# Performance work log

Hardware: AMD Instinct MI355X
Metric: run time of the kernel (lower is better)

## Reference

```python
import jax, jax.numpy as jnp
import numpy as np

ACT_BITS = 8
W_BITS = 8
BN_EPS = 1e-5


def _round_ste(x):
    # straight-through round (HAWQ-style ste_round)
    return x + jax.lax.stop_gradient(jnp.round(x) - x)


def _quant_sym(x, bits):
    # symmetric per-tensor fake quantization; scale treated as constant (EMA min/max in original)
    n = float(2 ** (bits - 1) - 1)
    s = jax.lax.stop_gradient(jnp.maximum(jnp.max(jnp.abs(x)) / n, 1e-8))
    xq = jnp.clip(_round_ste(x / s), -n - 1.0, n) * s
    return xq, s


def _conv(x, w, stride, pad):
    return jax.lax.conv_general_dilated(
        x, w, (stride, stride), [(pad, pad), (pad, pad)],
        dimension_numbers=("NCHW", "OIHW", "NCHW"))


def _quant_bn(x, gamma, beta, mean, var):
    # fold BN into a per-channel scale+bias; quantize the folded scale like a weight
    ws = gamma * jax.lax.rsqrt(var + BN_EPS)          # [C]
    wq, ws_scale = _quant_sym(ws, W_BITS)
    b = beta - mean * wq                               # [C]
    return x * wq[None, :, None, None] + b[None, :, None, None], ws_scale


def setup_inputs() -> dict:
    key = jax.random.key(0)
    ks = jax.random.split(key, 16)
    d = {}
    d["x"] = jax.random.normal(ks[0], (32, 128, 56, 56), jnp.float32)
    d["w1"] = jax.random.normal(ks[1], (256, 128, 3, 3), jnp.float32) * 0.05
    d["w2"] = jax.random.normal(ks[2], (256, 256, 3, 3), jnp.float32) * 0.05
    d["w_id"] = jax.random.normal(ks[3], (256, 128, 1, 1), jnp.float32) * 0.05
    for i, pfx in enumerate(["bn1", "bn2", "id"]):
        k4 = jax.random.split(ks[4 + i], 4)
        d[pfx + "_gamma"] = jax.random.uniform(k4[0], (256,), jnp.float32) + 0.5
        d[pfx + "_beta"] = jax.random.normal(k4[1], (256,), jnp.float32) * 0.1
        d[pfx + "_mean"] = jax.random.normal(k4[2], (256,), jnp.float32) * 0.1
        d[pfx + "_var"] = jax.random.uniform(k4[3], (256,), jnp.float32) + 0.5
    return d


def reference(x, w1, w2, w_id,
              bn1_gamma, bn1_beta, bn1_mean, bn1_var,
              bn2_gamma, bn2_beta, bn2_mean, bn2_var,
              id_gamma, id_beta, id_mean, id_var):
    # quant_act on block input
    xq, act_s = _quant_sym(x, ACT_BITS)

    # identity branch: 1x1 stride-2 quantized conv -> quant_act -> folded quant bn
    w_id_q, _ = _quant_sym(w_id, W_BITS)
    identity = _conv(xq, w_id_q, 2, 0)
    identity, _ = _quant_sym(identity, ACT_BITS)
    identity, _ = _quant_bn(identity, id_gamma, id_beta, id_mean, id_var)

    # main branch conv1 (3x3 stride 2) -> act quant -> bn -> relu -> act quant
    w1_q, _ = _quant_sym(w1, W_BITS)
    h = _conv(xq, w1_q, 2, 1)
    h, _ = _quant_sym(h, ACT_BITS)
    h, _ = _quant_bn(h, bn1_gamma, bn1_beta, bn1_mean, bn1_var)
    h = jax.nn.relu(h)
    h, _ = _quant_sym(h, ACT_BITS)

    # conv2 (3x3 stride 1) -> act quant -> bn
    w2_q, _ = _quant_sym(w2, W_BITS)
    h = _conv(h, w2_q, 1, 1)
    h, _ = _quant_sym(h, ACT_BITS)
    h, _ = _quant_bn(h, bn2_gamma, bn2_beta, bn2_mean, bn2_var)

    # residual add -> int32 requant -> relu
    h = h + identity
    h, out_s = _quant_sym(h, ACT_BITS)
    h = jax.nn.relu(h)
    return h, out_s
```

## Files before the change

kernel.cpp:

```cpp
#include <hip/hip_runtime.h>
#include <limits.h>

#define THREADS 256
#define GRID_BLOCKS 896

typedef int vi4 __attribute__((ext_vector_type(4)));

__device__ __forceinline__ float clamp8f(float q) { return fminf(fmaxf(q, -128.0f), 127.0f); }
__device__ __forceinline__ float sc_from_bits(unsigned b) {
  return fmaxf(__uint_as_float(b) / 127.0f, 1e-8f);
}
__device__ __forceinline__ signed char q8(float v, float s) {
  return (signed char)(int)clamp8f(rintf(v / s));
}


__device__ __forceinline__ void gbar(int* IS, int base, int bx, int subTgt) {
  asm volatile("s_waitcnt vmcnt(0)" ::: "memory");
  int old = __hip_atomic_fetch_add(IS + base + (bx & 7) * 16, 1, __ATOMIC_RELAXED,
                                   __HIP_MEMORY_SCOPE_AGENT);
  if (old == subTgt - 1) {
    int r = __hip_atomic_fetch_add(IS + base + 128, 1, __ATOMIC_RELAXED, __HIP_MEMORY_SCOPE_AGENT);
    if (r == 7)
      __hip_atomic_fetch_add(IS + base + 144, 1, __ATOMIC_RELAXED, __HIP_MEMORY_SCOPE_AGENT);
  }
  while (__hip_atomic_load(IS + base + 144, __ATOMIC_RELAXED, __HIP_MEMORY_SCOPE_SYSTEM) == 0)
    __builtin_amdgcn_s_sleep(2);
}

__device__ __forceinline__ void amax_body(const float4* __restrict__ p, int n4, int bid,
                                          int nblocks, int* __restrict__ slot) {
  const int tid = threadIdx.x;
  const int stride = nblocks * THREADS;
  float m = 0.0f;
  int i = bid * THREADS + tid;
  for (; i + 3 * stride < n4; i += 4 * stride) {
    float4 v0 = p[i];
    float4 v1 = p[i + stride];
    float4 v2 = p[i + 2 * stride];
    float4 v3 = p[i + 3 * stride];
    float m0 = fmaxf(fmaxf(fabsf(v0.x), fabsf(v0.y)), fmaxf(fabsf(v0.z), fabsf(v0.w)));
    float m1 = fmaxf(fmaxf(fabsf(v1.x), fabsf(v1.y)), fmaxf(fabsf(v1.z), fabsf(v1.w)));
    float m2 = fmaxf(fmaxf(fabsf(v2.x), fabsf(v2.y)), fmaxf(fabsf(v2.z), fabsf(v2.w)));
    float m3 = fmaxf(fmaxf(fabsf(v3.x), fabsf(v3.y)), fmaxf(fabsf(v3.z), fabsf(v3.w)));
    m = fmaxf(m, fmaxf(fmaxf(m0, m1), fmaxf(m2, m3)));
  }
  for (; i < n4; i += stride) {
    float4 v = p[i];
    m = fmaxf(m, fmaxf(fmaxf(fabsf(v.x), fabsf(v.y)), fmaxf(fabsf(v.z), fabsf(v.w))));
  }
#pragma unroll
  for (int k = 32; k >= 1; k >>= 1) m = fmaxf(m, __shfl_xor(m, k));
  __shared__ float wred[4];
  if ((tid & 63) == 0) wred[tid >> 6] = m;
  __syncthreads();
  if (tid == 0) {
    m = fmaxf(fmaxf(wred[0], wred[1]), fmaxf(wred[2], wred[3]));
    atomicMax(slot, __float_as_int(m));
  }
}

__device__ __forceinline__ float sc_slot(const int* IS, int slot) {
  unsigned u = (unsigned)__hip_atomic_load((int*)(IS + slot), __ATOMIC_RELAXED,
                                           __HIP_MEMORY_SCOPE_AGENT);
  return fmaxf(__uint_as_float(u) / 127.0f, 1e-8f);
}

__global__ __launch_bounds__(THREADS, 8) void k_pq(
    int* IS, const float* g1, const float* be1, const float* m1, const float* v1, float* wq1,
    float* b1, const float* g2, const float* be2, const float* m2, const float* v2, float* wq2,
    float* b2, const float* gi, const float* bei, const float* mi, const float* vvi, float* wqi,
    float* bi, const float* x, int* X8, const float* w1f, vi4* W1m, const float* w2f, vi4* W2m,
    const float* widf, vi4* Widm) {
  __shared__ signed char tile[56 * 132];
  __shared__ float red[THREADS];
  const int bx = blockIdx.x;
  const int t = threadIdx.x;

  {
    int b = bx;
    if (b < 3) {
      const float *gamma, *beta, *mean, *var;
      float *wq, *bb;
      if (b == 0) { gamma = g1; beta = be1; mean = m1; var = v1; wq = wq1; bb = b1; }
      else if (b == 1) { gamma = g2; beta = be2; mean = m2; var = v2; wq = wq2; bb = b2; }
      else { gamma = gi; beta = bei; mean = mi; var = vvi; wq = wqi; bb = bi; }
      int c = t;
      float ws = gamma[c] * (1.0f / sqrtf(var[c] + 1e-5f));
      red[c] = fabsf(ws);
      __syncthreads();
      for (int s = THREADS / 2; s > 0; s >>= 1) {
        if (c < s) red[c] = fmaxf(red[c], red[c + s]);
        __syncthreads();
      }
      float sws = fmaxf(red[0] / 127.0f, 1e-8f);
      float q = clamp8f(rintf(ws / sws)) * sws;
      wq[c] = q;
      bb[c] = beta[c] - mean[c] * q;
    } else {
      b -= 3;
      if (b < 64) {
        amax_body((const float4*)w1f, 73728, b, 64, IS + 1);
      } else {
        b -= 64;
        if (b < 128) {
          amax_body((const float4*)w2f, 147456, b, 128, IS + 2);
        } else {
          b -= 128;
          if (b < 16) amax_body((const float4*)widf, 8192, b, 16, IS + 3);
          else amax_body((const float4*)x, 3211264, b - 16, 1805, IS + 0);
        }
      }
    }
  }
  __syncthreads();
  if (t == 0) gbar(IS, 128, bx, 252);
  __syncthreads();

  int b = bx;
  if (b < 1792) {
    float s = sc_slot(IS, 0);
    int h = b % 56, n = b / 56;
    const float* xp = x + ((n * 128) * 56 + h) * 56;
#pragma unroll
    for (int k = 0; k < 28; ++k) {
      int i = t + k * 256;
      int w = i % 56, c = i / 56;
      tile[w * 132 + c] = q8(xp[c * 3136 + w], s);
    }
    __syncthreads();
    int* op = X8 + (n * 56 + h) * 56 * 32;
#pragma unroll
    for (int k = 0; k < 7; ++k) {
      int i = t + k * 256;
      int w = i >> 5, c4 = (i & 31) * 4;
      const signed char* tp = tile + w * 132 + c4;
      op[i] = (int)(unsigned char)tp[0] | ((int)(unsigned char)tp[1] << 8) |
              ((int)(unsigned char)tp[2] << 16) | ((int)(unsigned char)tp[3] << 24);
    }
    return;
  }
  if (b < 1864) {
    int tt = (b - 1792) * THREADS + t;
    float s = sc_slot(IS, 1);
    int lane = tt & 63;
    int cotile = (tt >> 6) & 15;
    int ks = tt >> 10;
    int tap = ks >> 1, kc = ks & 1;
    int kh = tap / 3, kw = tap % 3;
    int co = cotile * 16 + (lane & 15);
    int ci0 = kc * 64 + (lane >> 4) * 16;
    const float* src = w1f + (co * 128 + ci0) * 9 + kh * 3 + kw;
    int r[4];
#pragma unroll
    for (int q = 0; q < 4; ++q) {
      unsigned b0 = (unsigned char)q8(src[(q * 4 + 0) * 9], s);
      unsigned b1v = (unsigned char)q8(src[(q * 4 + 1) * 9], s);
      unsigned b2v = (unsigned char)q8(src[(q * 4 + 2) * 9], s);
      unsigned b3 = (unsigned char)q8(src[(q * 4 + 3) * 9], s);
      r[q] = (int)(b0 | (b1v << 8) | (b2v << 16) | (b3 << 24));
    }
    vi4 v = {r[0], r[1], r[2], r[3]};
    W1m[tt] = v;
    return;
  }
  if (b < 2008) {
    int tt = (b - 1864) * THREADS + t;
    float s = sc_slot(IS, 2);
    int lane = tt & 63;
    int cotile = (tt >> 6) & 15;
    int ks = tt >> 10;
    int tap = ks >> 2, kc = ks & 3;
    int kh = tap / 3, kw = tap % 3;
    int co = cotile * 16 + (lane & 15);
    int ci0 = kc * 64 + (lane >> 4) * 16;
    const float* src = w2f + (co * 256 + ci0) * 9 + kh * 3 + kw;
    int r[4];
#pragma unroll
    for (int q = 0; q < 4; ++q) {
      unsigned b0 = (unsigned char)q8(src[(q * 4 + 0) * 9], s);
      unsigned b1v = (unsigned char)q8(src[(q * 4 + 1) * 9], s);
      unsigned b2v = (unsigned char)q8(src[(q * 4 + 2) * 9], s);
      unsigned b3 = (unsigned char)q8(src[(q * 4 + 3) * 9], s);
      r[q] = (int)(b0 | (b1v << 8) | (b2v << 16) | (b3 << 24));
    }
    vi4 v = {r[0], r[1], r[2], r[3]};
    W2m[tt] = v;
    return;
  }
  {
    int tt = (b - 2008) * THREADS + t;
    float s = sc_slot(IS, 3);
    int lane = tt & 63;
    int cotile = (tt >> 6) & 15;
    int ks = tt >> 10;
    int co = cotile * 16 + (lane & 15);
    int ci0 = ks * 64 + (lane >> 4) * 16;
    const float* src = widf + co * 128 + ci0;
    int r[4];
#pragma unroll
    for (int q = 0; q < 4; ++q) {
      unsigned b0 = (unsigned char)q8(src[q * 4 + 0], s);
      unsigned b1v = (unsigned char)q8(src[q * 4 + 1], s);
      unsigned b2v = (unsigned char)q8(src[q * 4 + 2], s);
      unsigned b3 = (unsigned char)q8(src[q * 4 + 3], s);
      r[q] = (int)(b0 | (b1v << 8) | (b2v << 16) | (b3 << 24));
    }
    vi4 v = {r[0], r[1], r[2], r[3]};
    Widm[tt] = v;
  }
}

#define MFMA_I8(a, b, c) __builtin_amdgcn_mfma_i32_16x16x64_i8(a, b, c, 0, 0, 0)

__device__ __forceinline__ signed char qact(int v, float sxw, float s_h1, float s_y2, float wq,
                                            float bb) {
  float hf = (float)v * sxw;
  float q = clamp8f(rintf(hf / s_h1));
  float hv = q * s_h1;
  float y = fmaxf(hv * wq + bb, 0.0f);
  float a = fminf(fmaxf(rintf(y / s_y2), -128.0f), 127.0f);
  return (signed char)(int)a;
}

__global__ __launch_bounds__(THREADS, 4) void k_cv1(const int* X8, const vi4* __restrict__ W1m,
                                                    const vi4* __restrict__ Widm,
                                                    int* __restrict__ IDI, int* A2i, int* IS,
                                                    const float* __restrict__ wq1,
                                                    const float* __restrict__ b1, float* SC) {
  __shared__ __align__(16) int lds[9280];
  __shared__ int redA[4], redB[4];
  __shared__ float redF[4];
  __shared__ float sSxw, sSh1, sSy2;
  const int tid = threadIdx.x;
  const int bx = blockIdx.x;
  const int n = bx / 28, rr = bx % 28;
  const int hp = rr >> 1, nh = rr & 1;
  const int ho0 = hp * 2;
  vi4 zero = {0, 0, 0, 0};

  for (int r = 0; r < 5; ++r) {
    int h = 2 * ho0 - 1 + r;
    int* dst = lds + r * 58 * 32;
    if (h >= 0 && h < 56) {
      const vi4* src = (const vi4*)(X8 + (n * 56 + h) * 56 * 32);
      for (int i4 = tid; i4 < 448; i4 += THREADS) {
        int col = i4 >> 3, e0 = (i4 & 7) * 4;
        int cell = r * 58 + col + 1;
        *(vi4*)(lds + cell * 32 + (e0 ^ ((cell & 7) << 2))) = src[i4];
      }
      if (tid < 32) dst[tid] = 0;
      else if (tid >= 128 && tid < 160) dst[57 * 32 + (tid - 128)] = 0;
    } else {
      for (int i4 = tid; i4 < 464; i4 += THREADS) ((vi4*)dst)[i4] = zero;
    }
  }
  __syncthreads();

  const int lane = tid & 63, wv = tid >> 6;
  const int mw = wv & 1, nw = wv >> 1;
  const int lm = lane & 15, quad = lane >> 4;
  const int woc0 = lm, woc1 = (16 + lm) > 27 ? 27 : (16 + lm);
  const int choff = quad * 4;
  const int ho = ho0 + mw;
  const int obase = ((n * 28 + ho) * 28) * 256;
  const int ctbase = nh * 8 + nw * 4;

#define LDA(row, colp, sub)                                                              \
  (*(const vi4*)(lds + ((row) * 58 + (colp)) * 32 +                                      \
                 ((sub) ^ ((((row) * 58 + (colp)) & 7) << 2))))

  vi4 acc[2][4];
  vi4 bA[4], bB[4];
  vi4 a0A, a1A, a0B, a1B;

#pragma unroll
  for (int mt = 0; mt < 2; ++mt)
#pragma unroll
    for (int ct = 0; ct < 4; ++ct) acc[mt][ct] = zero;
  const vi4* wibase = Widm + ctbase * 64 + lane;
  {
    const int row = 2 * mw + 1;
#pragma unroll
    for (int kc = 0; kc < 2; ++kc) {
      vi4 a0 = LDA(row, 2 * woc0 + 1, kc * 16 + choff);
      vi4 a1 = LDA(row, 2 * woc1 + 1, kc * 16 + choff);
#pragma unroll
      for (int ct = 0; ct < 4; ++ct) {
        vi4 b = wibase[kc * 1024 + ct * 64];
        acc[0][ct] = MFMA_I8(a0, b, acc[0][ct]);
        acc[1][ct] = MFMA_I8(a1, b, acc[1][ct]);
      }
    }
  }
  int am = 0;
#pragma unroll
  for (int ct = 0; ct < 4; ++ct) {
    const int co = (ctbase + ct) * 16 + lm;
#pragma unroll
    for (int mt = 0; mt < 2; ++mt)
#pragma unroll
      for (int r = 0; r < 4; ++r) {
        int wo = mt * 16 + quad * 4 + r;
        if (wo < 28) {
          int v = acc[mt][ct][r];
          IDI[obase + wo * 256 + co] = v;
          am = max(am, v < 0 ? -v : v);
        }
      }
  }
#pragma unroll
  for (int k = 32; k >= 1; k >>= 1) am = max(am, __shfl_xor(am, k));
  if (lane == 0) redA[wv] = am;

#pragma unroll
  for (int mt = 0; mt < 2; ++mt)
#pragma unroll
    for (int ct = 0; ct < 4; ++ct) acc[mt][ct] = zero;
  const vi4* wbase = W1m + ctbase * 64 + lane;
#pragma unroll
  for (int ct = 0; ct < 4; ++ct) bA[ct] = wbase[ct * 64];
  {
    a0A = LDA(2 * mw, 2 * woc0, choff);
    a1A = LDA(2 * mw, 2 * woc1, choff);
  }
#pragma unroll 1
  for (int ks = 0; ks < 18; ks += 2) {
    {
      const int ksn = ks + 1;
      const int khn = (ksn >= 6) + (ksn >= 12);
      const int t2 = ksn - khn * 6;
      const int kwn = t2 >> 1, kcn = t2 & 1;
#pragma unroll
      for (int ct = 0; ct < 4; ++ct) bB[ct] = wbase[ksn * 1024 + ct * 64];
      const int row = 2 * mw + khn;
      a0B = LDA(row, 2 * woc0 + kwn, kcn * 16 + choff);
      a1B = LDA(row, 2 * woc1 + kwn, kcn * 16 + choff);
    }
#pragma unroll
    for (int ct = 0; ct < 4; ++ct) {
      acc[0][ct] = MFMA_I8(a0A, bA[ct], acc[0][ct]);
      acc[1][ct] = MFMA_I8(a1A, bA[ct], acc[1][ct]);
    }
    if (ks + 2 < 18) {
      const int ksn = ks + 2;
      const int khn = (ksn >= 6) + (ksn >= 12);
      const int t2 = ksn - khn * 6;
      const int kwn = t2 >> 1, kcn = t2 & 1;
#pragma unroll
      for (int ct = 0; ct < 4; ++ct) bA[ct] = wbase[ksn * 1024 + ct * 64];
      const int row = 2 * mw + khn;
      a0A = LDA(row, 2 * woc0 + kwn, kcn * 16 + choff);
      a1A = LDA(row, 2 * woc1 + kwn, kcn * 16 + choff);
    }
#pragma unroll
    for (int ct = 0; ct < 4; ++ct) {
      acc[0][ct] = MFMA_I8(a0B, bB[ct], acc[0][ct]);
      acc[1][ct] = MFMA_I8(a1B, bB[ct], acc[1][ct]);
    }
  }

  int vmx[4], vmn[4];
  int am1 = 0;
#pragma unroll
  for (int ct = 0; ct < 4; ++ct) {
    int vmax = INT_MIN, vmin = INT_MAX;
#pragma unroll
    for (int mt = 0; mt < 2; ++mt)
#pragma unroll
      for (int r = 0; r < 4; ++r) {
        int wo = mt * 16 + quad * 4 + r;
        if (wo < 28) {
          int v = acc[mt][ct][r];
          vmax = max(vmax, v);
          vmin = min(vmin, v);
        }
      }
    vmax = max(vmax, __shfl_xor(vmax, 16));
    vmax = max(vmax, __shfl_xor(vmax, 32));
    vmin = min(vmin, __shfl_xor(vmin, 16));
    vmin = min(vmin, __shfl_xor(vmin, 32));
    vmx[ct] = vmax;
    vmn[ct] = vmin;
    am1 = max(am1, max(vmax < 0 ? -vmax : vmax, vmin < 0 ? -vmin : vmin));
  }
#pragma unroll
  for (int k = 8; k >= 1; k >>= 1) am1 = max(am1, __shfl_xor(am1, k));
  if (lane == 0) redB[wv] = am1;

  __syncthreads();
#pragma unroll
  for (int ct = 0; ct < 4; ++ct) {
    const int cl = (nw * 4 + ct) * 16 + lm;
#pragma unroll
    for (int mt = 0; mt < 2; ++mt)
#pragma unroll
      for (int r = 0; r < 4; ++r) {
        int wo = mt * 16 + quad * 4 + r;
        if (wo < 28) lds[(mw * 28 + wo) * 130 + cl] = acc[mt][ct][r];
      }
  }
  if (tid == 0) {
    atomicMax(IS + 5, max(max(redA[0], redA[1]), max(redA[2], redA[3])));
    atomicMax(IS + 4, max(max(redB[0], redB[1]), max(redB[2], redB[3])));
    gbar(IS, 288, bx, 112);
    float sx = sc_slot(IS, 0);
    float sw1 = sc_slot(IS, 1);
    int mh1 = __hip_atomic_load(IS + 4, __ATOMIC_RELAXED, __HIP_MEMORY_SCOPE_AGENT);
    sSxw = sx * sw1;
    sSh1 = fmaxf(sSxw * (float)mh1 / 127.0f, 1e-8f);
  }
  __syncthreads();

  {
    const float sxw = sSxw, s_h1 = sSh1;
    float ym = 0.0f;
#pragma unroll
    for (int ct = 0; ct < 4; ++ct) {
      const int co = (ctbase + ct) * 16 + lm;
      float wq = wq1[co], bbc = b1[co];
      float q1 = clamp8f(rintf((float)vmx[ct] * sxw / s_h1));
      float q0 = clamp8f(rintf((float)vmn[ct] * sxw / s_h1));
      float y1 = fmaxf(q1 * s_h1 * wq + bbc, 0.0f);
      float y0 = fmaxf(q0 * s_h1 * wq + bbc, 0.0f);
      ym = fmaxf(ym, fmaxf(y1, y0));
    }
#pragma unroll
    for (int k = 8; k >= 1; k >>= 1) ym = fmaxf(ym, __shfl_xor(ym, k));
    if (lane == 0) redF[wv] = ym;
  }
  __syncthreads();
  if (tid == 0) {
    atomicMax(IS + 7, __float_as_int(fmaxf(fmaxf(redF[0], redF[1]), fmaxf(redF[2], redF[3]))));
    gbar(IS, 448, bx, 112);
    int mrf = __hip_atomic_load(IS + 7, __ATOMIC_RELAXED, __HIP_MEMORY_SCOPE_AGENT);
    float s_y2 = fmaxf(__int_as_float(mrf) / 127.0f, 1e-8f);
    sSy2 = s_y2;
    if (bx == 0) {
      int mid = __hip_atomic_load(IS + 5, __ATOMIC_RELAXED, __HIP_MEMORY_SCOPE_AGENT);
      float sx = sc_slot(IS, 0);
      float swid = sc_slot(IS, 3);
      SC[9] = s_y2;
      SC[10] = fmaxf(sx * swid * (float)mid / 127.0f, 1e-8f);
    }
  }
  __syncthreads();

  {
    const float sxw = sSxw, s_h1 = sSh1, s_y2 = sSy2;
#pragma unroll
    for (int k = 0; k < 7; ++k) {
      int i = tid + k * 256;
      int sp = i >> 5, c4i = i & 31;
      int mwp = sp >= 28 ? 1 : 0;
      int wo = sp - mwp * 28;
      int c0 = nh * 128 + c4i * 4;
      const int* pk = lds + sp * 130 + c4i * 4;
      unsigned r0 = (unsigned char)qact(pk[0], sxw, s_h1, s_y2, wq1[c0], b1[c0]);
      unsigned r1 = (unsigned char)qact(pk[1], sxw, s_h1, s_y2, wq1[c0 + 1], b1[c0 + 1]);
      unsigned r2 = (unsigned char)qact(pk[2], sxw, s_h1, s_y2, wq1[c0 + 2], b1[c0 + 2]);
      unsigned r3 = (unsigned char)qact(pk[3], sxw, s_h1, s_y2, wq1[c0 + 3], b1[c0 + 3]);
      A2i[((n * 28 + ho0 + mwp) * 28 + wo) * 64 + nh * 32 + c4i] =
          (int)(r0 | (r1 << 8) | (r2 << 16) | (r3 << 24));
    }
  }
#undef LDA
}

struct SumParams {
  float sxw2, s_h2, sxwid, s_idq;
};
__device__ __forceinline__ float sum_val(int v2, int vi, const SumParams& P, float wq2c, float b2c,
                                         float wqidc, float bidc) {
  float q2 = clamp8f(rintf((float)v2 * P.sxw2 / P.s_h2));
  float z = (q2 * P.s_h2) * wq2c + b2c;
  float qi = clamp8f(rintf((float)vi * P.sxwid / P.s_idq));
  float zi = (qi * P.s_idq) * wqidc + bidc;
  return z + zi;
}
__device__ __forceinline__ SumParams make_params2(const float* SC, const unsigned* ISu, int mh2) {
  SumParams P;
  float sx = sc_from_bits(ISu[0]);
  float sw2 = sc_from_bits(ISu[2]);
  float swid = sc_from_bits(ISu[3]);
  float s_y2 = SC[9];
  P.s_idq = SC[10];
  P.sxw2 = s_y2 * sw2;
  P.s_h2 = fmaxf(P.sxw2 * (float)mh2 / 127.0f, 1e-8f);
  P.sxwid = sx * swid;
  return P;
}

__global__ __launch_bounds__(THREADS, 4) void k_tail(const int* __restrict__ A2,
                                                     const vi4* __restrict__ W2m,
                                                     const int* __restrict__ IDI,
                                                     const float* SC, int* IS,
                                                     const float* __restrict__ wq2,
                                                     const float* __restrict__ b2,
                                                     const float* __restrict__ wqid,
                                                     const float* __restrict__ bidp,
                                                     float* __restrict__ out) {
  __shared__ __align__(16) int lds[4 * 30 * 68];
  __shared__ int redA[4];
  __shared__ float redF[4];
  __shared__ int sMh2;
  __shared__ float sOutS;
  const int tid = threadIdx.x;
  const int bx = blockIdx.x;
  const int n = bx / 28, rr = bx % 28;
  const int hp = rr >> 1, nh = rr & 1;
  const int ho0 = hp * 2;
  vi4 zero = {0, 0, 0, 0};

  for (int r = 0; r < 4; ++r) {
    int h = ho0 - 1 + r;
    int* dst = lds + r * 30 * 68;
    if (h >= 0 && h < 28) {
      const vi4* src = (const vi4*)(A2 + (n * 28 + h) * 28 * 64);
      for (int i4 = tid; i4 < 448; i4 += THREADS) {
        int col = i4 >> 4, c = (i4 & 15) * 4;
        *(vi4*)(dst + (col + 1) * 68 + c) = src[i4];
      }
      if (tid < 64) dst[tid] = 0;
      else if (tid >= 128 && tid < 192) dst[29 * 68 + (tid - 128)] = 0;
    } else {
      for (int i4 = tid; i4 < 510; i4 += THREADS) ((vi4*)dst)[i4] = zero;
    }
  }
  __syncthreads();

  const int lane = tid & 63, wv = tid >> 6;
  const int mw = wv & 1, nw = wv >> 1;
  const int lm = lane & 15, quad = lane >> 4;
  const int woc0 = lm, woc1 = (16 + lm) > 27 ? 27 : (16 + lm);
  const int choff = quad * 4;
  const int ctbase = nh * 8 + nw * 4;

  vi4 acc[2][4];
  vi4 bA[4], bB[4];
  vi4 a0A, a1A, a0B, a1B;
#pragma unroll
  for (int mt = 0; mt < 2; ++mt)
#pragma unroll
    for (int ct = 0; ct < 4; ++ct) acc[mt][ct] = zero;

  const vi4* wbase = W2m + ctbase * 64 + lane;
#pragma unroll
  for (int ct = 0; ct < 4; ++ct) bA[ct] = wbase[ct * 64];
  {
    const int ro = mw * 30;
    a0A = *(const vi4*)(lds + (ro + woc0) * 68 + choff);
    a1A = *(const vi4*)(lds + (ro + woc1) * 68 + choff);
  }
#pragma unroll 1
  for (int ks = 0; ks < 36; ks += 2) {
    {
      const int ksn = ks + 1;
      const int khn = (ksn >= 12) + (ksn >= 24);
      const int t2 = ksn - khn * 12;
      const int kwn = t2 >> 2, kcn = t2 & 3;
#pragma unroll
      for (int ct = 0; ct < 4; ++ct) bB[ct] = wbase[ksn * 1024 + ct * 64];
      const int ro = (mw + khn) * 30;
      a0B = *(const vi4*)(lds + (ro + woc0 + kwn) * 68 + kcn * 16 + choff);
      a1B = *(const vi4*)(lds + (ro + woc1 + kwn) * 68 + kcn * 16 + choff);
    }
#pragma unroll
    for (int ct = 0; ct < 4; ++ct) {
      acc[0][ct] = MFMA_I8(a0A, bA[ct], acc[0][ct]);
      acc[1][ct] = MFMA_I8(a1A, bA[ct], acc[1][ct]);
    }
    if (ks + 2 < 36) {
      const int ksn = ks + 2;
      const int khn = (ksn >= 12) + (ksn >= 24);
      const int t2 = ksn - khn * 12;
      const int kwn = t2 >> 2, kcn = t2 & 3;
#pragma unroll
      for (int ct = 0; ct < 4; ++ct) bA[ct] = wbase[ksn * 1024 + ct * 64];
      const int ro = (mw + khn) * 30;
      a0A = *(const vi4*)(lds + (ro + woc0 + kwn) * 68 + kcn * 16 + choff);
      a1A = *(const vi4*)(lds + (ro + woc1 + kwn) * 68 + kcn * 16 + choff);
    }
#pragma unroll
    for (int ct = 0; ct < 4; ++ct) {
      acc[0][ct] = MFMA_I8(a0B, bB[ct], acc[0][ct]);
      acc[1][ct] = MFMA_I8(a1B, bB[ct], acc[1][ct]);
    }
  }

  int am = 0;
#pragma unroll
  for (int ct = 0; ct < 4; ++ct)
#pragma unroll
    for (int mt = 0; mt < 2; ++mt)
#pragma unroll
      for (int r = 0; r < 4; ++r) {
        int wo = mt * 16 + quad * 4 + r;
        if (wo < 28) {
          int v = acc[mt][ct][r];
          am = max(am, v < 0 ? -v : v);
        }
      }
#pragma unroll
  for (int k = 32; k >= 1; k >>= 1) am = max(am, __shfl_xor(am, k));
  if (lane == 0) redA[wv] = am;
  __syncthreads();
  if (tid == 0) {
    int a = max(max(redA[0], redA[1]), max(redA[2], redA[3]));
    atomicMax(IS + 6, a);
  }

  int* sumsi = lds;
  float* sums = (float*)lds;
  const int ib = ((n * 28 + ho0) * 28) * 256 + nh * 128;
#pragma unroll
  for (int k = 0; k < 28; ++k) {
    int idx = tid + k * 256;
    int cl = idx & 127, sp = idx >> 7;
    sumsi[cl * 57 + sp] = IDI[ib + sp * 256 + cl];
  }
  __syncthreads();
  if (tid == 0) {
    gbar(IS, 608, bx, 112);
    sMh2 = __hip_atomic_load(IS + 6, __ATOMIC_RELAXED, __HIP_MEMORY_SCOPE_SYSTEM);
  }
  __syncthreads();
  const SumParams P = make_params2(SC, (const unsigned*)IS, sMh2);

  float fm = 0.0f;
#pragma unroll
  for (int ct = 0; ct < 4; ++ct) {
    const int co = (ctbase + ct) * 16 + lm;
    const int cl = co - nh * 128;
    float w2c = wq2[co], b2c = b2[co], wic = wqid[co], bic = bidp[co];
#pragma unroll
    for (int mt = 0; mt < 2; ++mt)
#pragma unroll
      for (int r = 0; r < 4; ++r) {
        int wo = mt * 16 + quad * 4 + r;
        if (wo < 28) {
          int slot = cl * 57 + mw * 28 + wo;
          float sv = sum_val(acc[mt][ct][r], sumsi[slot], P, w2c, b2c, wic, bic);
          sums[slot] = sv;
          fm = fmaxf(fm, fabsf(sv));
        }
      }
  }
#pragma unroll
  for (int k = 32; k >= 1; k >>= 1) fm = fmaxf(fm, __shfl_xor(fm, k));
  if (lane == 0) redF[wv] = fm;
  __syncthreads();
  if (tid == 0) {
    float a = fmaxf(fmaxf(redF[0], redF[1]), fmaxf(redF[2], redF[3]));
    atomicMax(IS + 11, __float_as_int(a));
    gbar(IS, 768, bx, 112);
    int mb = __hip_atomic_load(IS + 11, __ATOMIC_RELAXED, __HIP_MEMORY_SCOPE_SYSTEM);
    sOutS = fmaxf(__int_as_float(mb) / 127.0f, 1e-8f);
  }
  __syncthreads();
  const float out_s = sOutS;

  float* ob = out + n * 200704 + (nh * 128) * 784 + ho0 * 28;
#pragma unroll
  for (int k = 0; k < 28; ++k) {
    int idx = tid + k * 256;
    int cl = idx / 56, rem = idx % 56;
    float sv = sums[cl * 57 + rem];
    float q = clamp8f(rintf(sv / out_s));
    ob[cl * 784 + rem] = q > 0.0f ? q * out_s : 0.0f;
  }
  if (bx == 0 && tid == 0) out[6422528] = out_s;
}

extern "C" void kernel_launch(void* const* d_in, const int* in_sizes, int n_in, void* d_out,
                              int out_size, void* d_ws, size_t ws_size, hipStream_t stream) {
  (void)in_sizes; (void)n_in; (void)out_size; (void)ws_size;
  const float* x = (const float*)d_in[0];
  const float* w1 = (const float*)d_in[1];
  const float* w2 = (const float*)d_in[2];
  const float* wid = (const float*)d_in[3];
  const float* bn1g = (const float*)d_in[4];
  const float* bn1b = (const float*)d_in[5];
  const float* bn1m = (const float*)d_in[6];
  const float* bn1v = (const float*)d_in[7];
  const float* bn2g = (const float*)d_in[8];
  const float* bn2b = (const float*)d_in[9];
  const float* bn2m = (const float*)d_in[10];
  const float* bn2v = (const float*)d_in[11];
  const float* idg = (const float*)d_in[12];
  const float* idb = (const float*)d_in[13];
  const float* idm = (const float*)d_in[14];
  const float* idv = (const float*)d_in[15];

  char* ws = (char*)d_ws;
  float* SC = (float*)ws;
  int* IS = (int*)ws;
  float* wq1 = (float*)(ws + 4096);
  float* b1 = (float*)(ws + 5120);
  float* wq2 = (float*)(ws + 6144);
  float* b2 = (float*)(ws + 7168);
  float* wqid = (float*)(ws + 8192);
  float* bid = (float*)(ws + 9216);
  char* X8 = ws + 16384;
  char* A2 = X8;
  char* W1m = X8 + 12845056;
  char* W2m = W1m + 294912;
  char* Widm = W2m + 589824;
  int* IDI = (int*)(Widm + 32768);
  float* out = (float*)d_out;

  hipMemsetAsync(ws + 512, 0, 3584, stream);

  k_pq<<<2016, THREADS, 0, stream>>>(IS, bn1g, bn1b, bn1m, bn1v, wq1, b1, bn2g, bn2b, bn2m, bn2v,
                                     wq2, b2, idg, idb, idm, idv, wqid, bid, x, (int*)X8, w1,
                                     (vi4*)W1m, w2, (vi4*)W2m, wid, (vi4*)Widm);
  k_cv1<<<GRID_BLOCKS, THREADS, 0, stream>>>((const int*)X8, (const vi4*)W1m, (const vi4*)Widm,
                                             IDI, (int*)A2, IS, wq1, b1, SC);
  k_tail<<<GRID_BLOCKS, THREADS, 0, stream>>>((const int*)A2, (const vi4*)W2m, (const int*)IDI, SC,
                                              IS, wq2, b2, wqid, bid, out);
}
```

Measured before the change: 273.4 us.

## Split prep kernel at grid barrier into amax and quantize kernels, vectorize x loads

Replaces the single prep kernel's software grid barrier with a kernel boundary: one launch computes the BN folds and the abs-max reductions (x amax now uses 512 blocks), and a second launch quantizes and repacks x and the weights. This removes the 2016-block atomic barrier and its co-residency requirement, at the cost of an extra launch and a re-read of x. The x transpose-quantize loop now loads float4 and writes four LDS bytes per load, cutting the number of global load instructions.

```diff
diff --git a/kernel.cpp b/kernel.cpp
--- a/kernel.cpp
+++ b/kernel.cpp
@@ -66,67 +66,69 @@
   return fmaxf(__uint_as_float(u) / 127.0f, 1e-8f);
 }
 
-__global__ __launch_bounds__(THREADS, 8) void k_pq(
+__global__ __launch_bounds__(THREADS) void k_pre(
     int* IS, const float* g1, const float* be1, const float* m1, const float* v1, float* wq1,
     float* b1, const float* g2, const float* be2, const float* m2, const float* v2, float* wq2,
     float* b2, const float* gi, const float* bei, const float* mi, const float* vvi, float* wqi,
-    float* bi, const float* x, int* X8, const float* w1f, vi4* W1m, const float* w2f, vi4* W2m,
-    const float* widf, vi4* Widm) {
+    float* bi, const float4* w1, const float4* w2, const float4* wid, const float4* x) {
+  int b = blockIdx.x;
+  int c = threadIdx.x;
+  if (b < 3) {
+    const float *gamma, *beta, *mean, *var;
+    float *wq, *bb;
+    if (b == 0) { gamma = g1; beta = be1; mean = m1; var = v1; wq = wq1; bb = b1; }
+    else if (b == 1) { gamma = g2; beta = be2; mean = m2; var = v2; wq = wq2; bb = b2; }
+    else { gamma = gi; beta = bei; mean = mi; var = vvi; wq = wqi; bb = bi; }
+    __shared__ float red[THREADS];
+    float ws = gamma[c] * (1.0f / sqrtf(var[c] + 1e-5f));
+    red[c] = fabsf(ws);
+    __syncthreads();
+    for (int s = THREADS / 2; s > 0; s >>= 1) {
+      if (c < s) red[c] = fmaxf(red[c], red[c + s]);
+      __syncthreads();
+    }
+    float sws = fmaxf(red[0] / 127.0f, 1e-8f);
+    float q = clamp8f(rintf(ws / sws)) * sws;
+    wq[c] = q;
+    bb[c] = beta[c] - mean[c] * q;
+    return;
+  }
+  b -= 3;
+  if (b < 64) { amax_body(w1, 73728, b, 64, IS + 1); return; }
+  b -= 64;
+  if (b < 128) { amax_body(w2, 147456, b, 128, IS + 2); return; }
+  b -= 128;
+  if (b < 16) { amax_body(wid, 8192, b, 16, IS + 3); return; }
+  b -= 16;
+  amax_body(x, 3211264, b, 512, IS + 0);
+}
+
+__global__ __launch_bounds__(THREADS) void k_quant(const float* __restrict__ x,
+                                                   int* __restrict__ X8,
+                                                   const float* __restrict__ w1f,
+                                                   vi4* __restrict__ W1m,
+                                                   const float* __restrict__ w2f,
+                                                   vi4* __restrict__ W2m,
+                                                   const float* __restrict__ widf,
+                                                   vi4* __restrict__ Widm,
+                                                   const unsigned* __restrict__ ISu) {
   __shared__ signed char tile[56 * 132];
-  __shared__ float red[THREADS];
-  const int bx = blockIdx.x;
-  const int t = threadIdx.x;
-
-  {
-    int b = bx;
-    if (b < 3) {
-      const float *gamma, *beta, *mean, *var;
-      float *wq, *bb;
-      if (b == 0) { gamma = g1; beta = be1; mean = m1; var = v1; wq = wq1; bb = b1; }
-      else if (b == 1) { gamma = g2; beta = be2; mean = m2; var = v2; wq = wq2; bb = b2; }
-      else { gamma = gi; beta = bei; mean = mi; var = vvi; wq = wqi; bb = bi; }
-      int c = t;
-      float ws = gamma[c] * (1.0f / sqrtf(var[c] + 1e-5f));
-      red[c] = fabsf(ws);
-      __syncthreads();
-      for (int s = THREADS / 2; s > 0; s >>= 1) {
-        if (c < s) red[c] = fmaxf(red[c], red[c + s]);
-        __syncthreads();
-      }
-      float sws = fmaxf(red[0] / 127.0f, 1e-8f);
-      float q = clamp8f(rintf(ws / sws)) * sws;
-      wq[c] = q;
-      bb[c] = beta[c] - mean[c] * q;
-    } else {
-      b -= 3;
-      if (b < 64) {
-        amax_body((const float4*)w1f, 73728, b, 64, IS + 1);
-      } else {
-        b -= 64;
-        if (b < 128) {
-          amax_body((const float4*)w2f, 147456, b, 128, IS + 2);
-        } else {
-          b -= 128;
-          if (b < 16) amax_body((const float4*)widf, 8192, b, 16, IS + 3);
-          else amax_body((const float4*)x, 3211264, b - 16, 1805, IS + 0);
-        }
-      }
-    }
-  }
-  __syncthreads();
-  if (t == 0) gbar(IS, 128, bx, 252);
-  __syncthreads();
-
-  int b = bx;
+  int b = blockIdx.x;
+  int t = threadIdx.x;
   if (b < 1792) {
-    float s = sc_slot(IS, 0);
+    float s = sc_from_bits(ISu[0]);
     int h = b % 56, n = b / 56;
     const float* xp = x + ((n * 128) * 56 + h) * 56;
 #pragma unroll
-    for (int k = 0; k < 28; ++k) {
+    for (int k = 0; k < 7; ++k) {
       int i = t + k * 256;
-      int w = i % 56, c = i / 56;
-      tile[w * 132 + c] = q8(xp[c * 3136 + w], s);
+      int c = i / 14, w4 = i % 14;
+      float4 v = *(const float4*)(xp + c * 3136 + w4 * 4);
+      signed char* tp = &tile[(w4 * 4) * 132 + c];
+      tp[0] = q8(v.x, s);
+      tp[132] = q8(v.y, s);
+      tp[264] = q8(v.z, s);
+      tp[396] = q8(v.w, s);
     }
     __syncthreads();
     int* op = X8 + (n * 56 + h) * 56 * 32;
@@ -142,7 +144,7 @@
   }
   if (b < 1864) {
     int tt = (b - 1792) * THREADS + t;
-    float s = sc_slot(IS, 1);
+    float s = sc_from_bits(ISu[1]);
     int lane = tt & 63;
     int cotile = (tt >> 6) & 15;
     int ks = tt >> 10;
@@ -155,10 +157,10 @@
 #pragma unroll
     for (int q = 0; q < 4; ++q) {
       unsigned b0 = (unsigned char)q8(src[(q * 4 + 0) * 9], s);
-      unsigned b1v = (unsigned char)q8(src[(q * 4 + 1) * 9], s);
-      unsigned b2v = (unsigned char)q8(src[(q * 4 + 2) * 9], s);
+      unsigned b1 = (unsigned char)q8(src[(q * 4 + 1) * 9], s);
+      unsigned b2 = (unsigned char)q8(src[(q * 4 + 2) * 9], s);
       unsigned b3 = (unsigned char)q8(src[(q * 4 + 3) * 9], s);
-      r[q] = (int)(b0 | (b1v << 8) | (b2v << 16) | (b3 << 24));
+      r[q] = (int)(b0 | (b1 << 8) | (b2 << 16) | (b3 << 24));
     }
     vi4 v = {r[0], r[1], r[2], r[3]};
     W1m[tt] = v;
@@ -166,7 +168,7 @@
   }
   if (b < 2008) {
     int tt = (b - 1864) * THREADS + t;
-    float s = sc_slot(IS, 2);
+    float s = sc_from_bits(ISu[2]);
     int lane = tt & 63;
     int cotile = (tt >> 6) & 15;
     int ks = tt >> 10;
@@ -179,10 +181,10 @@
 #pragma unroll
     for (int q = 0; q < 4; ++q) {
       unsigned b0 = (unsigned char)q8(src[(q * 4 + 0) * 9], s);
-      unsigned b1v = (unsigned char)q8(src[(q * 4 + 1) * 9], s);
-      unsigned b2v = (unsigned char)q8(src[(q * 4 + 2) * 9], s);
+      unsigned b1 = (unsigned char)q8(src[(q * 4 + 1) * 9], s);
+      unsigned b2 = (unsigned char)q8(src[(q * 4 + 2) * 9], s);
       unsigned b3 = (unsigned char)q8(src[(q * 4 + 3) * 9], s);
-      r[q] = (int)(b0 | (b1v << 8) | (b2v << 16) | (b3 << 24));
+      r[q] = (int)(b0 | (b1 << 8) | (b2 << 16) | (b3 << 24));
     }
     vi4 v = {r[0], r[1], r[2], r[3]};
     W2m[tt] = v;
@@ -190,7 +192,7 @@
   }
   {
     int tt = (b - 2008) * THREADS + t;
-    float s = sc_slot(IS, 3);
+    float s = sc_from_bits(ISu[3]);
     int lane = tt & 63;
     int cotile = (tt >> 6) & 15;
     int ks = tt >> 10;
@@ -201,10 +203,10 @@
 #pragma unroll
     for (int q = 0; q < 4; ++q) {
       unsigned b0 = (unsigned char)q8(src[q * 4 + 0], s);
-      unsigned b1v = (unsigned char)q8(src[q * 4 + 1], s);
-      unsigned b2v = (unsigned char)q8(src[q * 4 + 2], s);
+      unsigned b1 = (unsigned char)q8(src[q * 4 + 1], s);
+      unsigned b2 = (unsigned char)q8(src[q * 4 + 2], s);
       unsigned b3 = (unsigned char)q8(src[q * 4 + 3], s);
-      r[q] = (int)(b0 | (b1v << 8) | (b2v << 16) | (b3 << 24));
+      r[q] = (int)(b0 | (b1 << 8) | (b2 << 16) | (b3 << 24));
     }
     vi4 v = {r[0], r[1], r[2], r[3]};
     Widm[tt] = v;
@@ -695,6 +697,7 @@
   char* ws = (char*)d_ws;
   float* SC = (float*)ws;
   int* IS = (int*)ws;
+  unsigned* ISu = (unsigned*)ws;
   float* wq1 = (float*)(ws + 4096);
   float* b1 = (float*)(ws + 5120);
   float* wq2 = (float*)(ws + 6144);
@@ -711,9 +714,11 @@
 
   hipMemsetAsync(ws + 512, 0, 3584, stream);
 
-  k_pq<<<2016, THREADS, 0, stream>>>(IS, bn1g, bn1b, bn1m, bn1v, wq1, b1, bn2g, bn2b, bn2m, bn2v,
-                                     wq2, b2, idg, idb, idm, idv, wqid, bid, x, (int*)X8, w1,
-                                     (vi4*)W1m, w2, (vi4*)W2m, wid, (vi4*)Widm);
+  k_pre<<<723, THREADS, 0, stream>>>(IS, bn1g, bn1b, bn1m, bn1v, wq1, b1, bn2g, bn2b, bn2m, bn2v,
+                                     wq2, b2, idg, idb, idm, idv, wqid, bid, (const float4*)w1,
+                                     (const float4*)w2, (const float4*)wid, (const float4*)x);
+  k_quant<<<2016, THREADS, 0, stream>>>(x, (int*)X8, w1, (vi4*)W1m, w2, (vi4*)W2m, wid,
+                                        (vi4*)Widm, ISu);
   k_cv1<<<GRID_BLOCKS, THREADS, 0, stream>>>((const int*)X8, (const vi4*)W1m, (const vi4*)Widm,
                                              IDI, (int*)A2, IS, wq1, b1, SC);
   k_tail<<<GRID_BLOCKS, THREADS, 0, stream>>>((const int*)A2, (const vi4*)W2m, (const int*)IDI, SC,
```

Measured after the change: 260.8 us. -4.6%, faster.

## Hold input rows in registers across grid barrier to avoid rereading x

Applied to the files above, without the earlier changes.

The prequant kernel now runs 896 persistent blocks, each loading two (n,h) rows of x into registers, computing the abs-max, crossing the grid barrier, then quantizing and transposing from registers. Previously x was read once for the amax pass and again after the barrier. Weight amax is now one float4 per wave, and weight repacking is spread across the first 64 threads of each block. This halves global reads of the large input but raises register pressure (56 floats per thread), lowers launch-bounds occupancy, and requires all 896 blocks to be co-resident for the barrier.

```diff
diff --git a/kernel.cpp b/kernel.cpp
--- a/kernel.cpp
+++ b/kernel.cpp
@@ -28,108 +28,175 @@
     __builtin_amdgcn_s_sleep(2);
 }
 
-__device__ __forceinline__ void amax_body(const float4* __restrict__ p, int n4, int bid,
-                                          int nblocks, int* __restrict__ slot) {
-  const int tid = threadIdx.x;
-  const int stride = nblocks * THREADS;
-  float m = 0.0f;
-  int i = bid * THREADS + tid;
-  for (; i + 3 * stride < n4; i += 4 * stride) {
-    float4 v0 = p[i];
-    float4 v1 = p[i + stride];
-    float4 v2 = p[i + 2 * stride];
-    float4 v3 = p[i + 3 * stride];
-    float m0 = fmaxf(fmaxf(fabsf(v0.x), fabsf(v0.y)), fmaxf(fabsf(v0.z), fabsf(v0.w)));
-    float m1 = fmaxf(fmaxf(fabsf(v1.x), fabsf(v1.y)), fmaxf(fabsf(v1.z), fabsf(v1.w)));
-    float m2 = fmaxf(fmaxf(fabsf(v2.x), fabsf(v2.y)), fmaxf(fabsf(v2.z), fabsf(v2.w)));
-    float m3 = fmaxf(fmaxf(fabsf(v3.x), fabsf(v3.y)), fmaxf(fabsf(v3.z), fabsf(v3.w)));
-    m = fmaxf(m, fmaxf(fmaxf(m0, m1), fmaxf(m2, m3)));
-  }
-  for (; i < n4; i += stride) {
-    float4 v = p[i];
-    m = fmaxf(m, fmaxf(fmaxf(fabsf(v.x), fabsf(v.y)), fmaxf(fabsf(v.z), fabsf(v.w))));
-  }
-#pragma unroll
-  for (int k = 32; k >= 1; k >>= 1) m = fmaxf(m, __shfl_xor(m, k));
-  __shared__ float wred[4];
-  if ((tid & 63) == 0) wred[tid >> 6] = m;
-  __syncthreads();
-  if (tid == 0) {
-    m = fmaxf(fmaxf(wred[0], wred[1]), fmaxf(wred[2], wred[3]));
-    atomicMax(slot, __float_as_int(m));
-  }
-}
-
 __device__ __forceinline__ float sc_slot(const int* IS, int slot) {
   unsigned u = (unsigned)__hip_atomic_load((int*)(IS + slot), __ATOMIC_RELAXED,
                                            __HIP_MEMORY_SCOPE_AGENT);
   return fmaxf(__uint_as_float(u) / 127.0f, 1e-8f);
 }
 
-__global__ __launch_bounds__(THREADS, 8) void k_pq(
+__global__ __launch_bounds__(THREADS, 4) void k_pq(
     int* IS, const float* g1, const float* be1, const float* m1, const float* v1, float* wq1,
     float* b1, const float* g2, const float* be2, const float* m2, const float* v2, float* wq2,
     float* b2, const float* gi, const float* bei, const float* mi, const float* vvi, float* wqi,
-    float* bi, const float* x, int* X8, const float* w1f, vi4* W1m, const float* w2f, vi4* W2m,
-    const float* widf, vi4* Widm) {
+    float* bi, const float* __restrict__ x, int* __restrict__ X8, const float* __restrict__ w1f,
+    vi4* __restrict__ W1m, const float* __restrict__ w2f, vi4* __restrict__ W2m,
+    const float* __restrict__ widf, vi4* __restrict__ Widm) {
   __shared__ signed char tile[56 * 132];
   __shared__ float red[THREADS];
+  __shared__ float wred[4];
+  __shared__ float sS[4];
   const int bx = blockIdx.x;
   const int t = threadIdx.x;
+  const int lane = t & 63, wv = t >> 6;
+
+  const int s0 = bx * 2;
+  const int n0 = s0 / 56, h0 = s0 % 56;
+  const int n1 = (s0 + 1) / 56, h1 = (s0 + 1) % 56;
+  const float* xp0 = x + ((n0 * 128) * 56 + h0) * 56;
+  const float* xp1 = x + ((n1 * 128) * 56 + h1) * 56;
+
+  float xs[56];
+#pragma unroll
+  for (int k = 0; k < 28; ++k) {
+    int i = t + k * 256;
+    xs[k] = xp0[(i / 56) * 3136 + (i % 56)];
+  }
+#pragma unroll
+  for (int k = 0; k < 28; ++k) {
+    int i = t + k * 256;
+    xs[28 + k] = xp1[(i / 56) * 3136 + (i % 56)];
+  }
+  float m = 0.0f;
+#pragma unroll
+  for (int k = 0; k < 56; ++k) m = fmaxf(m, fabsf(xs[k]));
 
   {
-    int b = bx;
-    if (b < 3) {
-      const float *gamma, *beta, *mean, *var;
-      float *wq, *bb;
-      if (b == 0) { gamma = g1; beta = be1; mean = m1; var = v1; wq = wq1; bb = b1; }
-      else if (b == 1) { gamma = g2; beta = be2; mean = m2; var = v2; wq = wq2; bb = b2; }
-      else { gamma = gi; beta = bei; mean = mi; var = vvi; wq = wqi; bb = bi; }
-      int c = t;
-      float ws = gamma[c] * (1.0f / sqrtf(var[c] + 1e-5f));
-      red[c] = fabsf(ws);
+    int wvg = bx * 4 + wv;
+    const float4* wp;
+    int* slot;
+    int g;
+    if (wvg < 1152) { wp = (const float4*)w1f; slot = IS + 1; g = wvg * 64 + lane; }
+    else if (wvg < 3456) { wp = (const float4*)w2f; slot = IS + 2; g = (wvg - 1152) * 64 + lane; }
+    else { wp = (const float4*)widf; slot = IS + 3; g = (wvg - 3456) * 64 + lane; }
+    float4 v = wp[g];
+    float wm = fmaxf(fmaxf(fabsf(v.x), fabsf(v.y)), fmaxf(fabsf(v.z), fabsf(v.w)));
+#pragma unroll
+    for (int k = 32; k >= 1; k >>= 1) wm = fmaxf(wm, __shfl_xor(wm, k));
+    if (lane == 0) atomicMax(slot, __float_as_int(wm));
+  }
+
+  if (bx < 3) {
+    const float *gamma, *beta, *mean, *var;
+    float *wq, *bb;
+    if (bx == 0) { gamma = g1; beta = be1; mean = m1; var = v1; wq = wq1; bb = b1; }
+    else if (bx == 1) { gamma = g2; beta = be2; mean = m2; var = v2; wq = wq2; bb = b2; }
+    else { gamma = gi; beta = bei; mean = mi; var = vvi; wq = wqi; bb = bi; }
+    float ws = gamma[t] * (1.0f / sqrtf(var[t] + 1e-5f));
+    red[t] = fabsf(ws);
+    __syncthreads();
+    for (int s = THREADS / 2; s > 0; s >>= 1) {
+      if (t < s) red[t] = fmaxf(red[t], red[t + s]);
       __syncthreads();
-      for (int s = THREADS / 2; s > 0; s >>= 1) {
-        if (c < s) red[c] = fmaxf(red[c], red[c + s]);
-        __syncthreads();
-      }
-      float sws = fmaxf(red[0] / 127.0f, 1e-8f);
-      float q = clamp8f(rintf(ws / sws)) * sws;
-      wq[c] = q;
-      bb[c] = beta[c] - mean[c] * q;
+    }
+    float sws = fmaxf(red[0] / 127.0f, 1e-8f);
+    float q = clamp8f(rintf(ws / sws)) * sws;
+    wq[t] = q;
+    bb[t] = beta[t] - mean[t] * q;
+  }
+
+#pragma unroll
+  for (int k = 32; k >= 1; k >>= 1) m = fmaxf(m, __shfl_xor(m, k));
+  if (lane == 0) wred[wv] = m;
+  __syncthreads();
+  if (t == 0) {
+    m = fmaxf(fmaxf(wred[0], wred[1]), fmaxf(wred[2], wred[3]));
+    atomicMax(IS + 0, __float_as_int(m));
+    gbar(IS, 128, bx, 112);
+    sS[0] = sc_slot(IS, 0);
+    sS[1] = sc_slot(IS, 1);
+    sS[2] = sc_slot(IS, 2);
+    sS[3] = sc_slot(IS, 3);
+  }
+  __syncthreads();
+
+  if (t < 64) {
+    int g = bx * 64 + t;
+    if (g < 18432) {
+      int tt = g;
+      float s = sS[1];
+      int lane2 = tt & 63;
+      int cotile = (tt >> 6) & 15;
+      int ks = tt >> 10;
+      int tap = ks >> 1, kc = ks & 1;
+      int kh = tap / 3, kw = tap % 3;
+      int co = cotile * 16 + (lane2 & 15);
+      int ci0 = kc * 64 + (lane2 >> 4) * 16;
+      const float* src = w1f + (co * 128 + ci0) * 9 + kh * 3 + kw;
+      int r[4];
+#pragma unroll
+      for (int q = 0; q < 4; ++q) {
+        unsigned b0 = (unsigned char)q8(src[(q * 4 + 0) * 9], s);
+        unsigned b1v = (unsigned char)q8(src[(q * 4 + 1) * 9], s);
+        unsigned b2v = (unsigned char)q8(src[(q * 4 + 2) * 9], s);
+        unsigned b3 = (unsigned char)q8(src[(q * 4 + 3) * 9], s);
+        r[q] = (int)(b0 | (b1v << 8) | (b2v << 16) | (b3 << 24));
+      }
+      vi4 v = {r[0], r[1], r[2], r[3]};
+      W1m[tt] = v;
+    } else if (g < 55296) {
+      int tt = g - 18432;
+      float s = sS[2];
+      int lane2 = tt & 63;
+      int cotile = (tt >> 6) & 15;
+      int ks = tt >> 10;
+      int tap = ks >> 2, kc = ks & 3;
+      int kh = tap / 3, kw = tap % 3;
+      int co = cotile * 16 + (lane2 & 15);
+      int ci0 = kc * 64 + (lane2 >> 4) * 16;
+      const float* src = w2f + (co * 256 + ci0) * 9 + kh * 3 + kw;
+      int r[4];
+#pragma unroll
+      for (int q = 0; q < 4; ++q) {
+        unsigned b0 = (unsigned char)q8(src[(q * 4 + 0) * 9], s);
+        unsigned b1v = (unsigned char)q8(src[(q * 4 + 1) * 9], s);
+        unsigned b2v = (unsigned char)q8(src[(q * 4 + 2) * 9], s);
+        unsigned b3 = (unsigned char)q8(src[(q * 4 + 3) * 9], s);
+        r[q] = (int)(b0 | (b1v << 8) | (b2v << 16) | (b3 << 24));
+      }
+      vi4 v = {r[0], r[1], r[2], r[3]};
+      W2m[tt] = v;
     } else {
-      b -= 3;
-      if (b < 64) {
-        amax_body((const float4*)w1f, 73728, b, 64, IS + 1);
-      } else {
-        b -= 64;
-        if (b < 128) {
-          amax_body((const float4*)w2f, 147456, b, 128, IS + 2);
-        } else {
-          b -= 128;
-          if (b < 16) amax_body((const float4*)widf, 8192, b, 16, IS + 3);
-          else amax_body((const float4*)x, 3211264, b - 16, 1805, IS + 0);
-        }
-      }
-    }
-  }
-  __syncthreads();
-  if (t == 0) gbar(IS, 128, bx, 252);
-  __syncthreads();
-
-  int b = bx;
-  if (b < 1792) {
-    float s = sc_slot(IS, 0);
-    int h = b % 56, n = b / 56;
-    const float* xp = x + ((n * 128) * 56 + h) * 56;
-#pragma unroll
-    for (int k = 0; k < 28; ++k) {
-      int i = t + k * 256;
-      int w = i % 56, c = i / 56;
-      tile[w * 132 + c] = q8(xp[c * 3136 + w], s);
-    }
-    __syncthreads();
-    int* op = X8 + (n * 56 + h) * 56 * 32;
+      int tt = g - 55296;
+      float s = sS[3];
+      int lane2 = tt & 63;
+      int cotile = (tt >> 6) & 15;
+      int ks = tt >> 10;
+      int co = cotile * 16 + (lane2 & 15);
+      int ci0 = ks * 64 + (lane2 >> 4) * 16;
+      const float* src = widf + co * 128 + ci0;
+      int r[4];
+#pragma unroll
+      for (int q = 0; q < 4; ++q) {
+        unsigned b0 = (unsigned char)q8(src[q * 4 + 0], s);
+        unsigned b1v = (unsigned char)q8(src[q * 4 + 1], s);
+        unsigned b2v = (unsigned char)q8(src[q * 4 + 2], s);
+        unsigned b3 = (unsigned char)q8(src[q * 4 + 3], s);
+        r[q] = (int)(b0 | (b1v << 8) | (b2v << 16) | (b3 << 24));
+      }
+      vi4 v = {r[0], r[1], r[2], r[3]};
+      Widm[tt] = v;
+    }
+  }
+
+  const float sx = sS[0];
+#pragma unroll
+  for (int k = 0; k < 28; ++k) {
+    int i = t + k * 256;
+    tile[(i % 56) * 132 + (i / 56)] = q8(xs[k], sx);
+  }
+  __syncthreads();
+  {
+    int* op = X8 + (n0 * 56 + h0) * 56 * 32;
 #pragma unroll
     for (int k = 0; k < 7; ++k) {
       int i = t + k * 256;
@@ -138,76 +205,24 @@
       op[i] = (int)(unsigned char)tp[0] | ((int)(unsigned char)tp[1] << 8) |
               ((int)(unsigned char)tp[2] << 16) | ((int)(unsigned char)tp[3] << 24);
     }
-    return;
-  }
-  if (b < 1864) {
-    int tt = (b - 1792) * THREADS + t;
-    float s = sc_slot(IS, 1);
-    int lane = tt & 63;
-    int cotile = (tt >> 6) & 15;
-    int ks = tt >> 10;
-    int tap = ks >> 1, kc = ks & 1;
-    int kh = tap / 3, kw = tap % 3;
-    int co = cotile * 16 + (lane & 15);
-    int ci0 = kc * 64 + (lane >> 4) * 16;
-    const float* src = w1f + (co * 128 + ci0) * 9 + kh * 3 + kw;
-    int r[4];
-#pragma unroll
-    for (int q = 0; q < 4; ++q) {
-      unsigned b0 = (unsigned char)q8(src[(q * 4 + 0) * 9], s);
-      unsigned b1v = (unsigned char)q8(src[(q * 4 + 1) * 9], s);
-      unsigned b2v = (unsigned char)q8(src[(q * 4 + 2) * 9], s);
-      unsigned b3 = (unsigned char)q8(src[(q * 4 + 3) * 9], s);
-      r[q] = (int)(b0 | (b1v << 8) | (b2v << 16) | (b3 << 24));
-    }
-    vi4 v = {r[0], r[1], r[2], r[3]};
-    W1m[tt] = v;
-    return;
-  }
-  if (b < 2008) {
-    int tt = (b - 1864) * THREADS + t;
-    float s = sc_slot(IS, 2);
-    int lane = tt & 63;
-    int cotile = (tt >> 6) & 15;
-    int ks = tt >> 10;
-    int tap = ks >> 2, kc = ks & 3;
-    int kh = tap / 3, kw = tap % 3;
-    int co = cotile * 16 + (lane & 15);
-    int ci0 = kc * 64 + (lane >> 4) * 16;
-    const float* src = w2f + (co * 256 + ci0) * 9 + kh * 3 + kw;
-    int r[4];
-#pragma unroll
-    for (int q = 0; q < 4; ++q) {
-      unsigned b0 = (unsigned char)q8(src[(q * 4 + 0) * 9], s);
-      unsigned b1v = (unsigned char)q8(src[(q * 4 + 1) * 9], s);
-      unsigned b2v = (unsigned char)q8(src[(q * 4 + 2) * 9], s);
-      unsigned b3 = (unsigned char)q8(src[(q * 4 + 3) * 9], s);
-      r[q] = (int)(b0 | (b1v << 8) | (b2v << 16) | (b3 << 24));
-    }
-    vi4 v = {r[0], r[1], r[2], r[3]};
-    W2m[tt] = v;
-    return;
-  }
+  }
+  __syncthreads();
+#pragma unroll
+  for (int k = 0; k < 28; ++k) {
+    int i = t + k * 256;
+    tile[(i % 56) * 132 + (i / 56)] = q8(xs[28 + k], sx);
+  }
+  __syncthreads();
   {
-    int tt = (b - 2008) * THREADS + t;
-    float s = sc_slot(IS, 3);
-    int lane = tt & 63;
-    int cotile = (tt >> 6) & 15;
-    int ks = tt >> 10;
-    int co = cotile * 16 + (lane & 15);
-    int ci0 = ks * 64 + (lane >> 4) * 16;
-    const float* src = widf + co * 128 + ci0;
-    int r[4];
-#pragma unroll
-    for (int q = 0; q < 4; ++q) {
-      unsigned b0 = (unsigned char)q8(src[q * 4 + 0], s);
-      unsigned b1v = (unsigned char)q8(src[q * 4 + 1], s);
-      unsigned b2v = (unsigned char)q8(src[q * 4 + 2], s);
-      unsigned b3 = (unsigned char)q8(src[q * 4 + 3], s);
-      r[q] = (int)(b0 | (b1v << 8) | (b2v << 16) | (b3 << 24));
-    }
-    vi4 v = {r[0], r[1], r[2], r[3]};
-    Widm[tt] = v;
+    int* op = X8 + (n1 * 56 + h1) * 56 * 32;
+#pragma unroll
+    for (int k = 0; k < 7; ++k) {
+      int i = t + k * 256;
+      int w = i >> 5, c4 = (i & 31) * 4;
+      const signed char* tp = tile + w * 132 + c4;
+      op[i] = (int)(unsigned char)tp[0] | ((int)(unsigned char)tp[1] << 8) |
+              ((int)(unsigned char)tp[2] << 16) | ((int)(unsigned char)tp[3] << 24);
+    }
   }
 }
 
@@ -711,9 +726,10 @@
 
   hipMemsetAsync(ws + 512, 0, 3584, stream);
 
-  k_pq<<<2016, THREADS, 0, stream>>>(IS, bn1g, bn1b, bn1m, bn1v, wq1, b1, bn2g, bn2b, bn2m, bn2v,
-                                     wq2, b2, idg, idb, idm, idv, wqid, bid, x, (int*)X8, w1,
-                                     (vi4*)W1m, w2, (vi4*)W2m, wid, (vi4*)Widm);
+  k_pq<<<GRID_BLOCKS, THREADS, 0, stream>>>(IS, bn1g, bn1b, bn1m, bn1v, wq1, b1, bn2g, bn2b,
+                                            bn2m, bn2v, wq2, b2, idg, idb, idm, idv, wqid, bid,
+                                            x, (int*)X8, w1, (vi4*)W1m, w2, (vi4*)W2m, wid,
+                                            (vi4*)Widm);
   k_cv1<<<GRID_BLOCKS, THREADS, 0, stream>>>((const int*)X8, (const vi4*)W1m, (const vi4*)Widm,
                                              IDI, (int*)A2, IS, wq1, b1, SC);
   k_tail<<<GRID_BLOCKS, THREADS, 0, stream>>>((const int*)A2, (const vi4*)W2m, (const int*)IDI, SC,
```

Result: slower. 314.5 us (+15.0%).
